# Optimization experiments

Hardware: AMD Instinct MI355X
Metric: run time of the kernel (lower is better)

The kernel has to match this reference:

```python
import jax, jax.numpy as jnp
import numpy as np

N_NODES = 40000
N_EDGES = 640000
C = 64
NUM_GAUSS = 50
RBF_STOP = 5.0


def silu(x):
    return x * jax.nn.sigmoid(x)


def setup_inputs() -> dict:
    key = jax.random.key(0)
    ks = jax.random.split(key, 16)
    scalar = jax.random.normal(ks[0], (N_NODES, C), dtype=jnp.float32)
    vector = jax.random.normal(ks[1], (N_NODES, 3, C), dtype=jnp.float32)
    position = jax.random.normal(ks[2], (N_NODES, 3), dtype=jnp.float32)
    # avoid self-edges so dist > 0 (sqrt grad finite in bwd variant)
    row = jax.random.randint(ks[3], (N_EDGES,), 0, N_NODES, dtype=jnp.int32)
    off = jax.random.randint(ks[4], (N_EDGES,), 1, N_NODES, dtype=jnp.int32)
    col = (row + off) % N_NODES
    edge_index = jnp.stack([row, col], axis=0)
    edge_attr = jax.random.uniform(ks[5], (N_EDGES,), dtype=jnp.float32) + 0.1
    s = 1.0 / np.sqrt(2 * C)
    Ws2s = jax.random.normal(ks[6], (2 * C, C), dtype=jnp.float32) * s
    bs2s = jnp.zeros((C,), dtype=jnp.float32)
    Wv2s = jax.random.normal(ks[7], (2 * C + NUM_GAUSS, C), dtype=jnp.float32) * s
    bv2s = jnp.zeros((C,), dtype=jnp.float32)
    Wsl = jax.random.normal(ks[8], (2 * C, C), dtype=jnp.float32) * s
    bsl = jnp.zeros((C,), dtype=jnp.float32)
    Ws2v = jax.random.normal(ks[9], (2 * C, C), dtype=jnp.float32) * s
    bs2v = jnp.zeros((C,), dtype=jnp.float32)
    Wv2v = jax.random.normal(ks[10], (2 * C, C), dtype=jnp.float32) * s
    Wvl = jax.random.normal(ks[11], (2 * C, C), dtype=jnp.float32) * s
    return dict(scalar=scalar, vector=vector, position=position,
                edge_index=edge_index, edge_attr=edge_attr,
                Ws2s=Ws2s, bs2s=bs2s, Wv2s=Wv2s, bv2s=bv2s,
                Wsl=Wsl, bsl=bsl, Ws2v=Ws2v, bs2v=bs2v, Wv2v=Wv2v, Wvl=Wvl)


def _molnet_layer(scalar, vector, position, edge_index, edge_attr,
                  Ws2s, bs2s, Wv2s, bv2s, Wsl, bsl, Ws2v, bs2v, Wv2v, Wvl):
    N = scalar.shape[0]
    row, col = edge_index[0], edge_index[1]
    # B=True degree normalization: deg[c] = sum of edge_attr into c
    deg = jax.ops.segment_sum(edge_attr, col, num_segments=N)
    dis = jnp.where(deg > 0, deg ** -0.5, 0.0)
    norm = dis[row] * dis[col] * edge_attr  # [E]

    # PyG convention: _i = target (col), _j = source (row)
    si, sj = scalar[col], scalar[row]          # [E, C]
    vi, vj = vector[col], vector[row]          # [E, 3, C]
    pi, pj = position[col], position[row]      # [E, 3]

    rel = pi - pj                              # [E, 3]
    dist = jnp.sqrt(jnp.sum(rel * rel, axis=-1))  # [E]

    # GaussianSmearing(0, 5, 50)
    offset = jnp.linspace(0.0, RBF_STOP, NUM_GAUSS, dtype=scalar.dtype)
    coeff = -0.5 / (RBF_STOP / (NUM_GAUSS - 1)) ** 2
    rbf = jnp.exp(coeff * (dist[:, None] - offset[None, :]) ** 2)  # [E, 50]

    # ---- Scalar_Conv message ----
    ss = silu(jnp.concatenate([si, sj], axis=1) @ Ws2s + bs2s)  # [E, C]
    vn_i = jnp.linalg.norm(vi, axis=1)  # [E, C], norm over 3-axis
    vn_j = jnp.linalg.norm(vj, axis=1)
    vs = silu(jnp.concatenate([vn_i, vn_j, rbf], axis=-1) @ Wv2s + bv2s)  # [E, C]
    msg_s = norm[:, None] * (jnp.concatenate([ss, vs], axis=1) @ Wsl + bsl)
    agg_s = jax.ops.segment_sum(msg_s, col, num_segments=N)  # [N, C]

    # ---- Vector_Conv message ----
    vv = jnp.concatenate([vi, vj], axis=-1) @ Wv2v  # [E, 3, C], no bias
    sv = jnp.tanh(jnp.concatenate([si, sj], axis=1) @ Ws2v + bs2v)  # [E, C]
    sv = sv[:, None, :] * rel[:, :, None]  # [E, 3, C]
    msg_v = norm[:, None, None] * (jnp.concatenate([vv, sv], axis=-1) @ Wvl)
    agg_v = jax.ops.segment_sum(msg_v, col, num_segments=N)  # [N, 3, C]

    scalar_out = silu(agg_s) + scalar
    vector_out = agg_v + vector
    return scalar_out, vector_out


def reference(scalar, vector, position, edge_index, edge_attr,
              Ws2s, bs2s, Wv2s, bv2s, Wsl, bsl, Ws2v, bs2v, Wv2v, Wvl):
    return _molnet_layer(scalar, vector, position, edge_index, edge_attr,
                         Ws2s, bs2s, Wv2s, bv2s, Wsl, bsl, Ws2v, bs2v, Wv2v, Wvl)
```

## Files before the change

kernel.cpp:

```cpp
#include <hip/hip_runtime.h>


typedef __attribute__((ext_vector_type(8))) short bf16x8;
typedef __attribute__((ext_vector_type(4))) float f32x4;
#define MFMA16(a, b, c) __builtin_amdgcn_mfma_f32_16x16x32_bf16(a, b, c, 0, 0, 0)

__device__ __forceinline__ unsigned short f2bf(float x) {
    union { float f; unsigned u; } v; v.f = x;
    unsigned r = v.u + 0x7FFF + ((v.u >> 16) & 1);
    return (unsigned short)(r >> 16);
}
__device__ __forceinline__ float bf2f(unsigned short h) {
    union { unsigned u; float f; } v; v.u = ((unsigned)h) << 16; return v.f;
}
__device__ __forceinline__ float ulo(unsigned u) {
    union { unsigned u; float f; } v; v.u = u << 16; return v.f;
}
__device__ __forceinline__ float uhi(unsigned u) {
    union { unsigned u; float f; } v; v.u = u & 0xffff0000u; return v.f;
}
__device__ __forceinline__ float silu_f(float x) {
    return x * __builtin_amdgcn_rcpf(1.0f + __expf(-x));
}
__device__ __forceinline__ float tanh_f(float x) {
    return 1.0f - 2.0f * __builtin_amdgcn_rcpf(1.0f + __expf(2.0f * x));
}
__device__ __forceinline__ int rfl(int x) { return __builtin_amdgcn_readfirstlane(x); }

__global__ __launch_bounds__(256) void deg_cnt_k(const int* __restrict__ ei,
                                                 const float* __restrict__ attr,
                                                 float* __restrict__ dc, int E) {
    int e = blockIdx.x * 256 + threadIdx.x;
    if (e < E) {
        int col = ei[E + e];
        atomicAdd(&dc[2 * col], attr[e]);
        atomicAdd((int*)dc + 2 * col + 1, 1);
    }
}

__global__ __launch_bounds__(1024) void scan1_k(const float* __restrict__ dc,
                                                int* __restrict__ blockSums, int N) {
    __shared__ int tmp[1024];
    int i = blockIdx.x * 1024 + threadIdx.x;
    tmp[threadIdx.x] = (i < N) ? ((const int*)dc)[2 * i + 1] : 0;
    __syncthreads();
    for (int s = 512; s > 0; s >>= 1) {
        if (threadIdx.x < s) tmp[threadIdx.x] += tmp[threadIdx.x + s];
        __syncthreads();
    }
    if (threadIdx.x == 0) blockSums[blockIdx.x] = tmp[0];
}

__global__ __launch_bounds__(1024) void scan3_k(const float* __restrict__ dc,
                                                const int* __restrict__ blockSums,
                                                int* __restrict__ offA,
                                                int* __restrict__ offB,
                                                float* __restrict__ dis, int N) {
    __shared__ int tmp[1024];
    __shared__ int base_s;
    if (threadIdx.x == 0) {
        int b = 0;
        for (int j = 0; j < (int)blockIdx.x; ++j) b += blockSums[j];
        base_s = b;
    }
    int i = blockIdx.x * 1024 + threadIdx.x;
    tmp[threadIdx.x] = (i < N) ? ((const int*)dc)[2 * i + 1] : 0;
    __syncthreads();
    for (int s = 1; s < 1024; s <<= 1) {
        int t = (threadIdx.x >= s) ? tmp[threadIdx.x - s] : 0;
        __syncthreads();
        tmp[threadIdx.x] += t;
        __syncthreads();
    }
    if (i < N) {
        int off = base_s + tmp[threadIdx.x];
        offA[i + 1] = off;
        offB[i + 1] = off;
        float d = dc[2 * i];
        dis[i] = (d > 0.0f) ? rsqrtf(d) : 0.0f;
    }
    if (blockIdx.x == 0 && threadIdx.x == 0) { offA[0] = 0; offB[0] = 0; }
}

__global__ __launch_bounds__(256) void mid_k(
    const int* __restrict__ ei, const float* __restrict__ attr,
    const float* __restrict__ pos,
    const float* __restrict__ dis, int* __restrict__ offA,
    float4* __restrict__ PLq, int E,
    const float* __restrict__ scalar, const float* __restrict__ vec,
    unsigned short* __restrict__ X, unsigned short* __restrict__ R2, int N,
    const float* __restrict__ Ws2s, const float* __restrict__ Ws2v,
    const float* __restrict__ Wv2s, const float* __restrict__ Wsl,
    const float* __restrict__ Wvl, const float* __restrict__ Wv2v,
    unsigned short* __restrict__ BT6, unsigned short* __restrict__ BTs,
    unsigned short* __restrict__ BTv, float* __restrict__ T2) {
    int idx = blockIdx.x * 256 + threadIdx.x;
    if (idx < E) {
        int row = ei[idx];
        int col = ei[E + idx];
        int p = atomicAdd(&offA[col], 1);
        float nrm = dis[col] * (dis[row] * attr[idx]);
        float r0 = pos[col * 3 + 0] - pos[row * 3 + 0];
        float r1 = pos[col * 3 + 1] - pos[row * 3 + 1];
        float r2 = pos[col * 3 + 2] - pos[row * 3 + 2];
        float d2 = r0 * r0 + r1 * r1 + r2 * r2;
        float t = fminf(sqrtf(d2) * (512.0f / 6.0f), 511.0f);
        PLq[2 * p]     = make_float4(__int_as_float(row * 192), nrm, r0, r1);
        PLq[2 * p + 1] = make_float4(r2, t, 0.0f, 0.0f);
        return;
    }
    idx -= E;
    if (idx < N * 64) {
        int n = idx >> 6, c = idx & 63;
        float v0 = vec[(size_t)n * 192 + c];
        float v1 = vec[(size_t)n * 192 + 64 + c];
        float v2 = vec[(size_t)n * 192 + 128 + c];
        X[(size_t)n * 128 + c] = f2bf(scalar[(size_t)n * 64 + c]);
        X[(size_t)n * 128 + 64 + c] = f2bf(sqrtf(v0 * v0 + v1 * v1 + v2 * v2));
        unsigned short* rb = R2 + (size_t)n * 384;
        rb[128 + 2 * c + 1] = f2bf(v0);
        *(unsigned*)(rb + 256 + 2 * c) =
            (unsigned)f2bf(v1) | ((unsigned)f2bf(v2) << 16);
        return;
    }
    idx -= N * 64;
    if (idx < 24576) {
        int y = idx >> 12, n = (idx >> 6) & 63, k = idx & 63;
        const float* W = (y < 2) ? Ws2s : (y < 4) ? Ws2v : Wv2s;
        int kk = (y & 1) ? (64 + k) : k;
        BT6[idx] = f2bf(W[kk * 64 + n]);
    } else if (idx < 32768) {
        int j = idx - 24576;
        int n = j >> 7, k = j & 127;
        BTs[(size_t)n * 128 + k] = f2bf(Wsl[k * 64 + n]);
    } else if (idx < 36864) {
        int j = idx - 32768;
        int n = j >> 6, k = j & 63;
        BTv[(size_t)n * 192 + k] = f2bf(Wvl[(64 + k) * 64 + n]);
    } else if (idx < 45056) {
        int j = idx - 36864;
        int half = j >> 12;
        int k = (j >> 6) & 63, c = j & 63;
        const float* Wr = Wv2v + (half ? 0 : 64 * 64) + k * 64;
        float acc = 0.0f;
        for (int m = 0; m < 64; ++m) acc += Wr[m] * Wvl[m * 64 + c];
        BTv[(size_t)c * 192 + (half ? 128 : 64) + k] = f2bf(acc);
    } else {
        int j = idx - 45056;
        if (j >= 513 * 64) return;
        int s = j >> 6, c = j & 63;
        float d = (float)s * (6.0f / 512.0f);
        float acc = 0.0f;
        for (int l = 0; l < 50; ++l) {
            float dl = d - 0.10204081632653061f * (float)l;
            acc += __expf(-48.02f * dl * dl) * Wv2s[(128 + l) * 64 + c];
        }
        T2[(s * 64 + c) * 2] = acc;
        if (s > 0) T2[((s - 1) * 64 + c) * 2 + 1] = acc;
    }
}

__global__ __launch_bounds__(256) void node_gemm_k(
    const unsigned short* __restrict__ X, const unsigned short* __restrict__ BT6,
    const float* __restrict__ bs2s, const float* __restrict__ bs2v,
    const float* __restrict__ bv2s,
    unsigned short* __restrict__ PC3, unsigned short* __restrict__ R2, int N) {
    const int lane = threadIdx.x & 63;
    const int mtile = blockIdx.x * 4 + (threadIdx.x >> 6);
    const int r0 = mtile * 16;
    if (r0 >= N) return;
    const int quad = lane >> 4, l = lane & 15;
    const int arow = min(r0 + l, N - 1);
    const unsigned short* ap = X + (size_t)arow * 128 + quad * 8;
    bf16x8 as0 = *(const bf16x8*)ap;
    bf16x8 as1 = *(const bf16x8*)(ap + 32);
    bf16x8 av0 = *(const bf16x8*)(ap + 64);
    bf16x8 av1 = *(const bf16x8*)(ap + 96);
    f32x4 acc[6][4];
#pragma unroll
    for (int y = 0; y < 6; ++y) {
        bf16x8 a0 = (y < 4) ? as0 : av0;
        bf16x8 a1 = (y < 4) ? as1 : av1;
        const unsigned short* bp = BT6 + (size_t)y * 4096 + (size_t)l * 64 + quad * 8;
#pragma unroll
        for (int nt = 0; nt < 4; ++nt) {
            acc[y][nt] = (f32x4){0.f, 0.f, 0.f, 0.f};
            bf16x8 b0 = *(const bf16x8*)(bp + nt * 1024);
            bf16x8 b1 = *(const bf16x8*)(bp + nt * 1024 + 32);
            acc[y][nt] = MFMA16(a0, b0, acc[y][nt]);
            acc[y][nt] = MFMA16(a1, b1, acc[y][nt]);
        }
    }
#pragma unroll
    for (int nt = 0; nt < 4; ++nt) {
        int col = nt * 16 + l;
        float b0 = bs2s[col], b1 = bs2v[col], b2 = bv2s[col];
#pragma unroll
        for (int i = 0; i < 4; ++i) {
            int row = r0 + quad * 4 + i;
            if (row < N) {
                unsigned short* pd = PC3 + (size_t)row * 192 + col * 3;
                pd[0] = f2bf(acc[0][nt][i] + b0);
                pd[1] = f2bf(acc[2][nt][i] + b1);
                pd[2] = f2bf(acc[4][nt][i] + b2);
                unsigned short* rd = R2 + (size_t)row * 384;
                *(unsigned*)(rd + 2 * col) =
                    (unsigned)f2bf(acc[1][nt][i]) |
                    ((unsigned)f2bf(acc[3][nt][i]) << 16);
                rd[128 + 2 * col] = f2bf(acc[5][nt][i]);
            }
        }
    }
}

#define STG(S, EIDX)                                                       \
    {                                                                      \
        const float4 pa_ = PLq[2 * (EIDX)];                                \
        const float4 pb_ = PLq[2 * (EIDX) + 1];                            \
        ro##S = rfl(__float_as_int(pa_.x));                                \
        nrm##S = pa_.y;                                                    \
        r0##S = pa_.z; r1##S = pa_.w; r2##S = pb_.x;                       \
        const unsigned* rp_ = R2u + ro##S;                                 \
        u0##S = rp_[lane]; u1##S = rp_[64 + lane]; u2##S = rp_[128 + lane];\
        int si_ = (int)pb_.y;                                              \
        fr##S = pb_.y - (float)si_;                                        \
        float2 tp_ = *(const float2*)(T2 + (si_ << 7) + lane2);            \
        tx##S = tp_.x; ty##S = tp_.y;                                      \
    }

#define CMP(S, NRMV)                                                       \
    {                                                                      \
        float ss_ = silu_f(pc0 + ulo(u0##S));                              \
        float tt_ = tanh_f(pc1 + uhi(u0##S));                              \
        float rb_ = tx##S + fr##S * (ty##S - tx##S);                       \
        float vs_ = silu_f(pc2 + ulo(u1##S) + rb_);                        \
        ws += NRMV;                                                        \
        a1 = fmaf(NRMV, ss_, a1);                                          \
        a2 = fmaf(NRMV, vs_, a2);                                          \
        float nt_ = NRMV * tt_;                                            \
        b30 = fmaf(nt_, r0##S, b30);                                       \
        b31 = fmaf(nt_, r1##S, b31);                                       \
        b32 = fmaf(nt_, r2##S, b32);                                       \
        bv0 = fmaf(NRMV, uhi(u1##S), bv0);                                 \
        bv1 = fmaf(NRMV, ulo(u2##S), bv1);                                 \
        bv2 = fmaf(NRMV, uhi(u2##S), bv2);                                 \
    }

#define TOTW 8192

__global__ __launch_bounds__(256) void edge_sorted_k(
    const unsigned short* __restrict__ PC3, const unsigned* __restrict__ R2u,
    const float* __restrict__ T2, const float4* __restrict__ PLq,
    const int* __restrict__ offB,
    unsigned short* __restrict__ Xs, unsigned short* __restrict__ Xv,
    float* __restrict__ Wsum, int N) {
    const int lane = threadIdx.x & 63;
    const int lane3 = lane * 3;
    const int lane2 = lane << 1;
    const int wave = rfl((blockIdx.x * 256 + threadIdx.x) >> 6);
#pragma unroll 1
    for (int col = wave; col < N; col += TOTW) {
        const int e0 = rfl(offB[col]);
        const int e1 = rfl(offB[col + 1]);
        const unsigned short* pcb = PC3 + (size_t)col * 192 + lane3;
        const float pc0 = bf2f(pcb[0]), pc1 = bf2f(pcb[1]), pc2 = bf2f(pcb[2]);
        const unsigned cd1 = R2u[(size_t)col * 192 + 64 + lane];
        const unsigned cd2 = R2u[(size_t)col * 192 + 128 + lane];
        const float wc0 = uhi(cd1), wc1 = ulo(cd2), wc2 = uhi(cd2);
        float a1 = 0, a2 = 0, ws = 0;
        float b30 = 0, b31 = 0, b32 = 0, bv0 = 0, bv1 = 0, bv2 = 0;
        if (e0 < e1) {
            int roA, roB;
            float nrmA, r0A, r1A, r2A, frA, txA, tyA;
            float nrmB, r0B, r1B, r2B, frB, txB, tyB;
            unsigned u0A, u1A, u2A, u0B, u1B, u2B;
            STG(A, e0);
            for (int e = e0; e < e1; e += 2) {
                const int eB = (e + 1 < e1) ? (e + 1) : e;
                STG(B, eB);
                const float nB = (e + 1 < e1) ? nrmB : 0.0f;
                CMP(A, nrmA);
                if (e + 2 < e1) STG(A, e + 2);
                CMP(B, nB);
            }
        }
        Xs[(size_t)col * 128 + lane] = f2bf(a1);
        Xs[(size_t)col * 128 + 64 + lane] = f2bf(a2);
        const size_t xb = (size_t)col * 576;
        Xv[xb + lane]       = f2bf(b30);
        Xv[xb + 64 + lane]  = f2bf(bv0);
        Xv[xb + 128 + lane] = f2bf(ws * wc0);
        Xv[xb + 192 + lane] = f2bf(b31);
        Xv[xb + 256 + lane] = f2bf(bv1);
        Xv[xb + 320 + lane] = f2bf(ws * wc1);
        Xv[xb + 384 + lane] = f2bf(b32);
        Xv[xb + 448 + lane] = f2bf(bv2);
        Xv[xb + 512 + lane] = f2bf(ws * wc2);
        if (lane == 0) Wsum[col] = ws;
    }
}
#undef STG
#undef CMP

__global__ __launch_bounds__(256) void gemm_sv_k(
    const unsigned short* __restrict__ Xs, const unsigned short* __restrict__ BTs,
    const unsigned short* __restrict__ Xv, const unsigned short* __restrict__ BTv,
    const float* __restrict__ bsl, const float* __restrict__ Wsum,
    const float* __restrict__ scalar, const float* __restrict__ vec,
    float* __restrict__ outs, float* __restrict__ outv, int N) {
    const int y = blockIdx.y;
    const int lane = threadIdx.x & 63;
    const int quad = lane >> 4, l = lane & 15;
    const int wave = threadIdx.x >> 6;
    if (y == 0) {
        const int r0 = (blockIdx.x * 4 + wave) * 16;
        if (r0 >= N) return;
        const int arow = min(r0 + l, N - 1);
        const unsigned short* aptr = Xs + (size_t)arow * 128 + quad * 8;
        bf16x8 a[4];
#pragma unroll
        for (int s = 0; s < 4; ++s) a[s] = *(const bf16x8*)(aptr + s * 32);
        const unsigned short* bptr = BTs + (size_t)l * 128 + quad * 8;
        f32x4 acc[4];
#pragma unroll
        for (int nt = 0; nt < 4; ++nt) {
            acc[nt] = (f32x4){0.f, 0.f, 0.f, 0.f};
#pragma unroll
            for (int s = 0; s < 4; ++s) {
                bf16x8 b = *(const bf16x8*)(bptr + (size_t)nt * 16 * 128 + s * 32);
                acc[nt] = MFMA16(a[s], b, acc[nt]);
            }
        }
#pragma unroll
        for (int nt = 0; nt < 4; ++nt) {
            int col = nt * 16 + l;
            float bc = bsl[col];
#pragma unroll
            for (int i = 0; i < 4; ++i) {
                int row = r0 + quad * 4 + i;
                if (row < N) {
                    float wsn = Wsum[row];
                    outs[(size_t)row * 64 + col] =
                        silu_f(acc[nt][i] + wsn * bc) + scalar[(size_t)row * 64 + col];
                }
            }
        }
    } else {
        const int M = 3 * N;
        const int r0 = ((y - 1) * (N / 16) + blockIdx.x * 4 + wave) * 16;
        if (r0 >= M) return;
        const int arow = min(r0 + l, M - 1);
        const unsigned short* aptr = Xv + (size_t)arow * 192 + quad * 8;
        bf16x8 a[6];
#pragma unroll
        for (int s = 0; s < 6; ++s) a[s] = *(const bf16x8*)(aptr + s * 32);
        const unsigned short* bptr = BTv + (size_t)l * 192 + quad * 8;
        f32x4 acc[4];
#pragma unroll
        for (int nt = 0; nt < 4; ++nt) {
            acc[nt] = (f32x4){0.f, 0.f, 0.f, 0.f};
#pragma unroll
            for (int s = 0; s < 6; ++s) {
                bf16x8 b = *(const bf16x8*)(bptr + (size_t)nt * 16 * 192 + s * 32);
                acc[nt] = MFMA16(a[s], b, acc[nt]);
            }
        }
#pragma unroll
        for (int nt = 0; nt < 4; ++nt) {
            int col = nt * 16 + l;
#pragma unroll
            for (int i = 0; i < 4; ++i) {
                int row = r0 + quad * 4 + i;
                if (row < M)
                    outv[(size_t)row * 64 + col] = acc[nt][i] + vec[(size_t)row * 64 + col];
            }
        }
    }
}

extern "C" void kernel_launch(void* const* d_in, const int* in_sizes, int n_in,
                              void* d_out, int out_size, void* d_ws, size_t ws_size,
                              hipStream_t stream) {
    const float* scalar     = (const float*)d_in[0];
    const float* vector     = (const float*)d_in[1];
    const float* position   = (const float*)d_in[2];
    const int*   edge_index = (const int*)d_in[3];
    const float* edge_attr  = (const float*)d_in[4];
    const float* Ws2s       = (const float*)d_in[5];
    const float* bs2s       = (const float*)d_in[6];
    const float* Wv2s       = (const float*)d_in[7];
    const float* bv2s       = (const float*)d_in[8];
    const float* Wsl        = (const float*)d_in[9];
    const float* bsl        = (const float*)d_in[10];
    const float* Ws2v       = (const float*)d_in[11];
    const float* bs2v       = (const float*)d_in[12];
    const float* Wv2v       = (const float*)d_in[13];
    const float* Wvl        = (const float*)d_in[14];

    const int N = in_sizes[0] / 64;
    const int E = in_sizes[3] / 2;
    const size_t sN = (size_t)N;
    const int nb = (N + 1023) / 1024;

    float* W = (float*)d_ws;
    float*          dis  = W;
    unsigned short* X    = (unsigned short*)(W + sN);
    unsigned short* Xs   = X;
    unsigned short* R2   = (unsigned short*)(W + 65 * sN);
    unsigned short* PC3  = (unsigned short*)(W + 257 * sN);
    unsigned short* Xv   = (unsigned short*)(W + 353 * sN);
    float* dc        = W + 353 * sN;
    int*   offA      = (int*)(W + 355 * sN);
    int*   blockSums = (int*)(W + 357 * sN);
    unsigned short* BT6 = (unsigned short*)(W + 358 * sN);
    float* Wsum = W + 641 * sN;
    int*   offB = (int*)(W + 642 * sN);
    unsigned short* BTs = (unsigned short*)(W + 644 * sN);
    unsigned short* BTv = (unsigned short*)(W + 644 * sN + 4096);
    float* T2   = W + 644 * sN + 10240;

    float* outs = (float*)d_out;
    float* outv = outs + 64 * sN;
    float4* PLq = (float4*)d_out;

    hipMemsetAsync(dc, 0, sizeof(float) * 2 * sN, stream);

    deg_cnt_k<<<(E + 255) / 256, 256, 0, stream>>>(edge_index, edge_attr, dc, E);
    scan1_k<<<nb, 1024, 0, stream>>>(dc, blockSums, N);
    scan3_k<<<nb, 1024, 0, stream>>>(dc, blockSums, offA, offB, dis, N);

    const int midTot = E + N * 64 + 45056 + 513 * 64;
    mid_k<<<(midTot + 255) / 256, 256, 0, stream>>>(
        edge_index, edge_attr, position, dis, offA, PLq, E,
        scalar, vector, X, R2, N,
        Ws2s, Ws2v, Wv2s, Wsl, Wvl, Wv2v, BT6, BTs, BTv, T2);

    const int mtilesN = (N + 15) / 16;
    node_gemm_k<<<(mtilesN + 3) / 4, 256, 0, stream>>>(
        X, BT6, bs2s, bs2v, bv2s, PC3, R2, N);

    edge_sorted_k<<<TOTW / 4, 256, 0, stream>>>(
        PC3, (const unsigned*)R2, T2, PLq, offB, Xs, Xv, Wsum, N);

    gemm_sv_k<<<dim3((mtilesN + 3) / 4, 4), 256, 0, stream>>>(
        Xs, BTs, Xv, BTv, bsl, Wsum, scalar, vector, outs, outv, N);
}
```

Measured before the change: 375.8 us.

## Pack degree sum and count into one 64-bit atomic; dynamic per-block column queue

The degree pass now packs a fixed-point edge_attr sum and an edge count into a single 64-bit atomicAdd per edge, where it previously issued two 32-bit atomics. The edge aggregation kernel changes from a static grid-stride over columns to 1024-thread blocks that each own a contiguous range of columns. Waves inside a block claim columns through a shared-memory atomic counter, which balances uneven in-degree. The trade-off is that the fixed-point sum loses some precision relative to float accumulation, and the block count and occupancy pattern both change.

```diff
diff --git a/kernel.cpp b/kernel.cpp
--- a/kernel.cpp
+++ b/kernel.cpp
@@ -27,22 +27,26 @@
 }
 __device__ __forceinline__ int rfl(int x) { return __builtin_amdgcn_readfirstlane(x); }
 
+#define SUM_MASK ((1ULL << 44) - 1)
+
 __global__ __launch_bounds__(256) void deg_cnt_k(const int* __restrict__ ei,
                                                  const float* __restrict__ attr,
-                                                 float* __restrict__ dc, int E) {
+                                                 unsigned long long* __restrict__ dc,
+                                                 int E) {
     int e = blockIdx.x * 256 + threadIdx.x;
     if (e < E) {
         int col = ei[E + e];
-        atomicAdd(&dc[2 * col], attr[e]);
-        atomicAdd((int*)dc + 2 * col + 1, 1);
-    }
-}
-
-__global__ __launch_bounds__(1024) void scan1_k(const float* __restrict__ dc,
+        unsigned long long pk = (1ULL << 44) |
+            (unsigned long long)(unsigned)__float2uint_rn(attr[e] * 16777216.0f);
+        atomicAdd(&dc[col], pk);
+    }
+}
+
+__global__ __launch_bounds__(1024) void scan1_k(const unsigned long long* __restrict__ dc,
                                                 int* __restrict__ blockSums, int N) {
     __shared__ int tmp[1024];
     int i = blockIdx.x * 1024 + threadIdx.x;
-    tmp[threadIdx.x] = (i < N) ? ((const int*)dc)[2 * i + 1] : 0;
+    tmp[threadIdx.x] = (i < N) ? (int)(dc[i] >> 44) : 0;
     __syncthreads();
     for (int s = 512; s > 0; s >>= 1) {
         if (threadIdx.x < s) tmp[threadIdx.x] += tmp[threadIdx.x + s];
@@ -51,7 +55,7 @@
     if (threadIdx.x == 0) blockSums[blockIdx.x] = tmp[0];
 }
 
-__global__ __launch_bounds__(1024) void scan3_k(const float* __restrict__ dc,
+__global__ __launch_bounds__(1024) void scan3_k(const unsigned long long* __restrict__ dc,
                                                 const int* __restrict__ blockSums,
                                                 int* __restrict__ offA,
                                                 int* __restrict__ offB,
@@ -64,7 +68,8 @@
         base_s = b;
     }
     int i = blockIdx.x * 1024 + threadIdx.x;
-    tmp[threadIdx.x] = (i < N) ? ((const int*)dc)[2 * i + 1] : 0;
+    unsigned long long dcv = (i < N) ? dc[i] : 0ULL;
+    tmp[threadIdx.x] = (int)(dcv >> 44);
     __syncthreads();
     for (int s = 1; s < 1024; s <<= 1) {
         int t = (threadIdx.x >= s) ? tmp[threadIdx.x - s] : 0;
@@ -76,7 +81,7 @@
         int off = base_s + tmp[threadIdx.x];
         offA[i + 1] = off;
         offB[i + 1] = off;
-        float d = dc[2 * i];
+        float d = (float)(dcv & SUM_MASK) * 5.9604645e-08f;
         dis[i] = (d > 0.0f) ? rsqrtf(d) : 0.0f;
     }
     if (blockIdx.x == 0 && threadIdx.x == 0) { offA[0] = 0; offB[0] = 0; }
@@ -246,23 +251,27 @@
         bv2 = fmaf(NRMV, uhi(u2##S), bv2);                                 \
     }
 
-#define TOTW 8192
-
-__global__ __launch_bounds__(256) void edge_sorted_k(
+__global__ __launch_bounds__(1024) void edge_sorted_k(
     const unsigned short* __restrict__ PC3, const unsigned* __restrict__ R2u,
     const float* __restrict__ T2, const float4* __restrict__ PLq,
     const int* __restrict__ offB,
     unsigned short* __restrict__ Xs, unsigned short* __restrict__ Xv,
-    float* __restrict__ Wsum, int N) {
+    float* __restrict__ Wsum, int N, int CPB) {
+    __shared__ int qidx;
+    if (threadIdx.x == 0) qidx = 0;
+    __syncthreads();
     const int lane = threadIdx.x & 63;
-    const int lane3 = lane * 3;
     const int lane2 = lane << 1;
-    const int wave = rfl((blockIdx.x * 256 + threadIdx.x) >> 6);
-#pragma unroll 1
-    for (int col = wave; col < N; col += TOTW) {
+    const int c0 = blockIdx.x * CPB;
+    const int cend = min(c0 + CPB, N);
+    for (int it = 0; it <= CPB; ++it) {
+        int t_ = 0;
+        if (lane == 0) t_ = atomicAdd(&qidx, 1);
+        const int col = c0 + rfl(t_);
+        if (col >= cend) break;
         const int e0 = rfl(offB[col]);
         const int e1 = rfl(offB[col + 1]);
-        const unsigned short* pcb = PC3 + (size_t)col * 192 + lane3;
+        const unsigned short* pcb = PC3 + (size_t)col * 192 + lane * 3;
         const float pc0 = bf2f(pcb[0]), pc1 = bf2f(pcb[1]), pc2 = bf2f(pcb[2]);
         const unsigned cd1 = R2u[(size_t)col * 192 + 64 + lane];
         const unsigned cd2 = R2u[(size_t)col * 192 + 128 + lane];
@@ -409,7 +418,7 @@
     unsigned short* R2   = (unsigned short*)(W + 65 * sN);
     unsigned short* PC3  = (unsigned short*)(W + 257 * sN);
     unsigned short* Xv   = (unsigned short*)(W + 353 * sN);
-    float* dc        = W + 353 * sN;
+    unsigned long long* dc = (unsigned long long*)(W + 353 * sN);
     int*   offA      = (int*)(W + 355 * sN);
     int*   blockSums = (int*)(W + 357 * sN);
     unsigned short* BT6 = (unsigned short*)(W + 358 * sN);
@@ -423,7 +432,7 @@
     float* outv = outs + 64 * sN;
     float4* PLq = (float4*)d_out;
 
-    hipMemsetAsync(dc, 0, sizeof(float) * 2 * sN, stream);
+    hipMemsetAsync(dc, 0, sizeof(unsigned long long) * sN, stream);
 
     deg_cnt_k<<<(E + 255) / 256, 256, 0, stream>>>(edge_index, edge_attr, dc, E);
     scan1_k<<<nb, 1024, 0, stream>>>(dc, blockSums, N);
@@ -439,8 +448,11 @@
     node_gemm_k<<<(mtilesN + 3) / 4, 256, 0, stream>>>(
         X, BT6, bs2s, bs2v, bv2s, PC3, R2, N);
 
-    edge_sorted_k<<<TOTW / 4, 256, 0, stream>>>(
-        PC3, (const unsigned*)R2, T2, PLq, offB, Xs, Xv, Wsum, N);
+    const int NB  = 512;
+    const int CPB = (N + NB - 1) / NB;
+    const int nblk = (N + CPB - 1) / CPB;
+    edge_sorted_k<<<nblk, 1024, 0, stream>>>(
+        PC3, (const unsigned*)R2, T2, PLq, offB, Xs, Xv, Wsum, N, CPB);
 
     gemm_sv_k<<<dim3((mtilesN + 3) / 4, 4), 256, 0, stream>>>(
         Xs, BTs, Xv, BTv, bsl, Wsum, scalar, vector, outs, outv, N);
```

Measured after the change: 344.6 us. -8.3%, faster.
